# Optimization experiments

Measured on AMD Instinct MI355X. Metric: run time of the kernel, lower is better.

The kernel has to match this reference:

```python
import jax, jax.numpy as jnp
import numpy as np

N_ENT = 100000
N_REL = 500
D_IN = 128
D_OUT = 128
E_HALF = 1000000  # edges per direction; edge_index has 2*E_HALF columns
BN_EPS = 1e-5


def ccorr(a, b):
    # circular correlation: irfft(conj(rfft(a)) * rfft(b))
    d = a.shape[-1]
    return jnp.fft.irfft(jnp.conj(jnp.fft.rfft(a, axis=-1)) * jnp.fft.rfft(b, axis=-1), n=d, axis=-1)


def setup_inputs() -> dict:
    key = jax.random.key(0)
    ks = jax.random.split(key, 12)
    inv = 1.0 / np.sqrt(D_IN)
    inp = {
        "x": jax.random.normal(ks[0], (N_ENT, D_IN), dtype=jnp.float32),
        "rel_embed": jax.random.normal(ks[1], (N_REL, D_IN), dtype=jnp.float32),
        "w_in": jax.random.uniform(ks[2], (D_IN, D_OUT), minval=-inv, maxval=inv, dtype=jnp.float32),
        "w_out": jax.random.uniform(ks[3], (D_IN, D_OUT), minval=-inv, maxval=inv, dtype=jnp.float32),
        "w_loop": jax.random.uniform(ks[4], (D_IN, D_OUT), minval=-inv, maxval=inv, dtype=jnp.float32),
        "w_rel": jax.random.uniform(ks[5], (D_IN, D_OUT), minval=-inv, maxval=inv, dtype=jnp.float32),
        "loop_rel": jax.random.normal(ks[6], (1, D_IN), dtype=jnp.float32),
        "bias": jnp.zeros((D_OUT,), dtype=jnp.float32),
        "bn_weight": jnp.ones((D_OUT,), dtype=jnp.float32),
        "bn_bias": jnp.zeros((D_OUT,), dtype=jnp.float32),
        "edge_index": jax.random.randint(ks[7], (2, 2 * E_HALF), 0, N_ENT, dtype=jnp.int32),
        "edge_type": jax.random.randint(ks[8], (2 * E_HALF,), 0, N_REL, dtype=jnp.int32),
    }
    return inp


def _compute_norm(edge_index, num_ent):
    row, col = edge_index[0], edge_index[1]
    ones = jnp.ones(row.shape, dtype=jnp.float32)
    deg = jax.ops.segment_sum(ones, row, num_segments=num_ent)
    deg_inv = jnp.where(deg > 0, jax.lax.rsqrt(jnp.maximum(deg, 1.0)), 0.0)
    return deg_inv[row] * deg_inv[col]  # [E]


def _propagate(x, edge_index, edge_type, rel_all, weight, norm, num_ent):
    x_j = x[edge_index[0]]              # [E, d_in] gather source nodes
    r = rel_all[edge_type]              # [E, d_in] gather relation embeds
    m = ccorr(x_j, r) @ weight          # [E, d_out]
    if norm is not None:
        m = m * norm[:, None]
    return jax.ops.segment_sum(m, edge_index[1], num_segments=num_ent)


def reference(x, rel_embed, w_in, w_out, w_loop, w_rel, loop_rel, bias, bn_weight, bn_bias, edge_index, edge_type):
    num_ent = x.shape[0]
    rel_all = jnp.concatenate([rel_embed, loop_rel], axis=0)  # [R+1, d_in]
    e = edge_index.shape[1] // 2
    in_idx, out_idx = edge_index[:, :e], edge_index[:, e:]
    in_type, out_type = edge_type[:e], edge_type[e:]

    in_norm = _compute_norm(in_idx, num_ent)
    out_norm = _compute_norm(out_idx, num_ent)

    in_res = _propagate(x, in_idx, in_type, rel_all, w_in, in_norm, num_ent)
    out_res = _propagate(x, out_idx, out_type, rel_all, w_out, out_norm, num_ent)
    # loop edges are (i, i) with relation = last row of rel_all -> identity scatter
    loop_res = ccorr(x, rel_all[-1][None, :]) @ w_loop

    out = (in_res + out_res + loop_res) * (1.0 / 3.0) + bias
    # BatchNorm1d (training-mode batch statistics, biased variance)
    mu = jnp.mean(out, axis=0)
    var = jnp.mean((out - mu) ** 2, axis=0)
    out = (out - mu) * jax.lax.rsqrt(var + BN_EPS) * bn_weight + bn_bias

    rel_out = (rel_all @ w_rel)[:-1]
    return out, rel_out
```

## Files before the change

### kernel.cpp

```cpp
#include <hip/hip_runtime.h>
#include <cmath>

#define N_ENT 100000
#define EHALF 1000000
#define N_REL 500
#define NBUK 196
#define DPB 512
#define SCAP 7680
#define DCAP 6656

#ifndef M_PI
#define M_PI 3.14159265358979323846
#endif

typedef _Float16 f16x8 __attribute__((ext_vector_type(8)));
typedef _Float16 f16x4 __attribute__((ext_vector_type(4)));
typedef _Float16 f16x2 __attribute__((ext_vector_type(2)));
typedef float f32x4 __attribute__((ext_vector_type(4)));

union H16 { unsigned short u; _Float16 h; };

__global__ void k_tabs(float* __restrict__ Ftab, float* __restrict__ Gtab,
                       _Float16* __restrict__ FtabT) {
  int i = blockIdx.x * 256 + threadIdx.x;
  if (i >= 128 * 128) return;
  int n = i >> 7, s = i & 127;
  float fv, gv;
  if (s == 0) { fv = 1.f; gv = 1.f / 384.f; }
  else if (s == 1) { float sg = (n & 1) ? -1.f : 1.f; fv = sg; gv = sg / 384.f; }
  else {
    int f = s >> 1;
    double ang = 2.0 * M_PI * (double)((f * n) & 127) / 128.0;
    if (!(s & 1)) { double c = cos(ang); fv = (float)c; gv = (float)(c * (2.0 / 384.0)); }
    else { double sv = sin(ang); fv = (float)(-sv); gv = (float)(-sv * (2.0 / 384.0)); }
  }
  Ftab[n * 128 + s] = fv;
  Gtab[s * 128 + n] = gv;
  FtabT[s * 128 + n] = (_Float16)fv;
}

__global__ void k_dftrel(const float* __restrict__ rel, const float* __restrict__ looprel,
                         const float* __restrict__ Ftab, float* __restrict__ Rf,
                         _Float16* __restrict__ RfL) {
  __shared__ float sv[128];
  int r = blockIdx.x, s = threadIdx.x;
  const float* row = (r < N_REL) ? rel + (size_t)r * 128 : looprel;
  float acc = 0.f;
  for (int n = 0; n < 128; ++n) acc += row[n] * Ftab[n * 128 + s];
  Rf[(size_t)r * 128 + s] = acc;
  sv[s] = acc;
  __syncthreads();
  if (s < 64) {
    f16x4 o;
    if (s == 0) {
      o = (f16x4){(_Float16)sv[0], (_Float16)0.f, (_Float16)0.f, (_Float16)sv[1]};
    } else {
      float rx = sv[2 * s], ry = sv[2 * s + 1];
      o = (f16x4){(_Float16)rx, (_Float16)ry, (_Float16)ry, (_Float16)(-rx)};
    }
    ((f16x4*)RfL)[(size_t)r * 64 + s] = o;
  }
}

__global__ void k_rotloop(float* __restrict__ Wl, const float* __restrict__ Rfl) {
  int c = threadIdx.x;
  int f = blockIdx.x;
  if (f == 0) {
    Wl[c]       = Rfl[0] * Wl[c];
    Wl[128 + c] = Rfl[1] * Wl[128 + c];
  } else {
    float rr = Rfl[2 * f], ri = Rfl[2 * f + 1];
    float a = Wl[2 * f * 128 + c], b = Wl[(2 * f + 1) * 128 + c];
    Wl[2 * f * 128 + c]       = rr * a + ri * b;
    Wl[(2 * f + 1) * 128 + c] = ri * a - rr * b;
  }
}

__global__ void k_wt(const float* __restrict__ W, _Float16* __restrict__ WT, int K) {
  int i = blockIdx.x * 256 + threadIdx.x;
  if (i >= K * 128) return;
  int k = i >> 7, c = i & 127;
  WT[(size_t)c * K + k] = (_Float16)W[i];
}

__global__ __launch_bounds__(256) void gemm128(
    const float* __restrict__ A, int lda,
    const float* __restrict__ B,
    float* __restrict__ C, int ldc,
    int M, int K) {
  __shared__ float As[64][64];
  __shared__ float Bs[64][128];
  const int t = threadIdx.x;
  const int m0 = blockIdx.x * 64;
  const int cg = t & 31;
  const int eg = t >> 5;
  float acc[8][4];
#pragma unroll
  for (int i = 0; i < 8; ++i)
#pragma unroll
    for (int j = 0; j < 4; ++j) acc[i][j] = 0.f;

  for (int k0 = 0; k0 < K; k0 += 64) {
#pragma unroll
    for (int p = 0; p < 4; ++p) {
      int idx = t + p * 256;
      int r = idx >> 4, c4 = idx & 15;
      int gr = m0 + r;
      float4 v = make_float4(0.f, 0.f, 0.f, 0.f);
      if (gr < M) v = *(const float4*)(A + (size_t)gr * lda + k0 + c4 * 4);
      *(float4*)&As[r][c4 * 4] = v;
    }
#pragma unroll
    for (int p = 0; p < 8; ++p) {
      int idx = t + p * 256;
      int r = idx >> 5, c4 = idx & 31;
      float4 v = *(const float4*)(B + (size_t)(k0 + r) * 128 + c4 * 4);
      *(float4*)&Bs[r][c4 * 4] = v;
    }
    __syncthreads();
#pragma unroll
    for (int k = 0; k < 64; ++k) {
      float4 bv = *(float4*)&Bs[k][cg * 4];
#pragma unroll
      for (int i = 0; i < 8; ++i) {
        float av = As[eg * 8 + i][k];
        acc[i][0] += av * bv.x; acc[i][1] += av * bv.y;
        acc[i][2] += av * bv.z; acc[i][3] += av * bv.w;
      }
    }
    __syncthreads();
  }
#pragma unroll
  for (int i = 0; i < 8; ++i) {
    int gr = m0 + eg * 8 + i;
    if (gr < M) {
      float4 v = make_float4(acc[i][0], acc[i][1], acc[i][2], acc[i][3]);
      *(float4*)(C + (size_t)gr * ldc + cg * 4) = v;
    }
  }
}

__device__ inline f16x8 loadAfrag(const _Float16* A, size_t off) {
  return *(const f16x8*)(A + off);
}
__device__ inline f16x8 loadAfrag(const float* A, size_t off) {
  float4 u = *(const float4*)(A + off);
  float4 v = *(const float4*)(A + off + 4);
  return (f16x8){(_Float16)u.x, (_Float16)u.y, (_Float16)u.z, (_Float16)u.w,
                 (_Float16)v.x, (_Float16)v.y, (_Float16)v.z, (_Float16)v.w};
}

template<int K, int KS, int MODE, bool BN, typename AT>
__global__ __launch_bounds__(256) void mgemm(
    const AT* __restrict__ A, int lda,
    const _Float16* __restrict__ BT,
    void* __restrict__ Cv, int ldc, int M,
    const float* __restrict__ bias, float* __restrict__ bnAcc) {
  __shared__ __align__(16) char lds[128 * KS * 2 + 4096];
  const int t = threadIdx.x;
  const int l = t & 63, w = t >> 6;
  const int col0 = l & 15, rg = l >> 4;
  const int rowbase = blockIdx.x * 256 + w * 64;
  const int sw = (col0 & 7) << 4;

  f32x4 acc[4][8];
  f32x4 zz = {0.f, 0.f, 0.f, 0.f};
#pragma unroll
  for (int a = 0; a < 4; ++a)
#pragma unroll
    for (int n = 0; n < 8; ++n) acc[a][n] = zz;

  for (int ks0 = 0; ks0 < K; ks0 += KS) {
    __syncthreads();
    const int CH = KS / 8;
    for (int u = t; u < 128 * CH; u += 256) {
      int col = u / CH, kc = u % CH;
      f16x8 vch = *(const f16x8*)(BT + (size_t)col * K + ks0 + kc * 8);
      *(f16x8*)(lds + col * (KS * 2) + ((kc * 16) ^ ((col & 7) << 4))) = vch;
    }
    __syncthreads();
#pragma unroll
    for (int ks = 0; ks < KS / 32; ++ks) {
      int kb = ks0 + ks * 32 + rg * 8;
      f16x8 af[4];
#pragma unroll
      for (int a = 0; a < 4; ++a) {
        int rb = rowbase + a * 16;
        if (rb < M) af[a] = loadAfrag(A, (size_t)(rb + col0) * lda + kb);
        else af[a] = (f16x8){0, 0, 0, 0, 0, 0, 0, 0};
      }
      int kc = ks * 4 + rg;
#pragma unroll
      for (int n = 0; n < 8; ++n) {
        f16x8 bf = *(const f16x8*)(lds + (n * 16 + col0) * (KS * 2) + ((kc * 16) ^ sw));
#pragma unroll
        for (int a = 0; a < 4; ++a)
          acc[a][n] = __builtin_amdgcn_mfma_f32_16x16x32_f16(af[a], bf, acc[a][n], 0, 0, 0);
      }
    }
  }

  if (MODE == 1) {
    _Float16* C = (_Float16*)Cv;
#pragma unroll
    for (int a = 0; a < 4; ++a) {
      int rb = rowbase + a * 16;
      if (rb >= M) continue;
#pragma unroll
      for (int r = 0; r < 4; ++r) {
        int row = rb + rg * 4 + r;
#pragma unroll
        for (int n = 0; n < 8; ++n) {
          int col = n * 16 + col0;
          C[(size_t)row * ldc + col] = (_Float16)acc[a][n][r];
        }
      }
    }
  } else {
    float* C = (float*)Cv;
    float sacc[8], qacc[8];
#pragma unroll
    for (int n = 0; n < 8; ++n) { sacc[n] = 0.f; qacc[n] = 0.f; }
#pragma unroll
    for (int a = 0; a < 4; ++a) {
      int rb = rowbase + a * 16;
      if (rb >= M) continue;
#pragma unroll
      for (int n = 0; n < 8; ++n) {
        int col = n * 16 + col0;
        float bi = bias ? bias[col] : 0.f;
#pragma unroll
        for (int r = 0; r < 4; ++r) {
          float val = acc[a][n][r] + bi;
          C[(size_t)(rb + rg * 4 + r) * ldc + col] = val;
          if (BN) { sacc[n] += val; qacc[n] += val * val; }
        }
      }
    }
    if (BN) {
      __syncthreads();
      float* Sb = (float*)lds;
      float* Qb = Sb + 512;
#pragma unroll
      for (int n = 0; n < 8; ++n) {
        float s = sacc[n], q = qacc[n];
        s += __shfl_xor(s, 16); s += __shfl_xor(s, 32);
        q += __shfl_xor(q, 16); q += __shfl_xor(q, 32);
        if (rg == 0) { Sb[w * 128 + n * 16 + col0] = s; Qb[w * 128 + n * 16 + col0] = q; }
      }
      __syncthreads();
      if (t < 128) {
        float s = Sb[t] + Sb[128 + t] + Sb[256 + t] + Sb[384 + t];
        float q = Qb[t] + Qb[128 + t] + Qb[256 + t] + Qb[384 + t];
        atomicAdd(&bnAcc[t], s);
        atomicAdd(&bnAcc[128 + t], q);
      }
    }
  }
}

__global__ void k_init(int* __restrict__ gSI, int* __restrict__ gSO,
                       int* __restrict__ gDI, int* __restrict__ gDO) {
  int t = threadIdx.x;
  if (t < NBUK) {
    gSI[t] = t * SCAP; gSO[t] = t * SCAP;
    gDI[t] = t * DCAP; gDO[t] = t * DCAP;
  }
}

__global__ __launch_bounds__(256) void k_splitS2(
    const int* __restrict__ ei,
    int* __restrict__ gSI, int* __restrict__ gSO,
    unsigned* __restrict__ recSI, unsigned* __restrict__ recSO) {
  __shared__ int bcnt[NBUK], cnt2[NBUK], base[NBUK], nn[NBUK];
  const int t = threadIdx.x;
  const int dir = blockIdx.x >> 8;
  const int blk = blockIdx.x & 255;
  const int* key = ei + (dir ? EHALF : 0);
  int* gcur = dir ? gSO : gSI;
  unsigned* rec = dir ? recSO : recSI;
  const int SPAN = 3907;
  int st = blk * SPAN;
  int en = min(st + SPAN, EHALF);
  if (t < NBUK) { bcnt[t] = 0; cnt2[t] = 0; }
  __syncthreads();
  unsigned rr[16]; int bb[16];
#pragma unroll
  for (int j = 0; j < 16; ++j) {
    int e = st + j * 256 + t;
    bb[j] = -1;
    if (e < en) {
      int s = key[e];
      rr[j] = (unsigned)(s & 511) | 0x80000000u;
      int b = s >> 9;
      bb[j] = b;
      atomicAdd(&bcnt[b], 1);
    }
  }
  __syncthreads();
  if (t < NBUK) {
    int n = bcnt[t]; nn[t] = n;
    base[t] = n ? atomicAdd(&gcur[t], (n + 7) & ~7) : 0;
  }
  __syncthreads();
#pragma unroll
  for (int j = 0; j < 16; ++j) {
    if (bb[j] >= 0) {
      int p = atomicAdd(&cnt2[bb[j]], 1);
      rec[(size_t)base[bb[j]] + p] = rr[j];
    }
  }
  __syncthreads();
  if (t < NBUK) {
    int n = nn[t];
    if (n & 7) {
      int pe = (n + 7) & ~7;
      for (int k = n; k < pe; ++k) rec[(size_t)base[t] + k] = 0u;
    }
  }
}

__global__ __launch_bounds__(512) void k_dhist(
    const unsigned* __restrict__ recI, const int* __restrict__ gI,
    float* __restrict__ dinvIn,
    const unsigned* __restrict__ recO, const int* __restrict__ gO,
    float* __restrict__ dinvOut) {
  int b = blockIdx.x % NBUK;
  int dir = blockIdx.x / NBUK;
  const unsigned* rec = dir ? recO : recI;
  const int gs = b * SCAP;
  const int ge = (dir ? gO : gI)[b];
  float* dinv = dir ? dinvOut : dinvIn;
  __shared__ int h[DPB];
  int t = threadIdx.x;
  h[t] = 0;
  __syncthreads();
  for (int i = gs + t; i < ge; i += 512) {
    unsigned r = rec[i];
    if (r >> 31) atomicAdd(&h[r & 511], 1);
  }
  __syncthreads();
  int ent = b * 512 + t;
  if (ent < N_ENT) {
    int d = h[t];
    dinv[ent] = (d > 0) ? rsqrtf((float)d) : 0.f;
  }
}

__global__ __launch_bounds__(256) void k_splitD2(
    const int* __restrict__ ei, const int* __restrict__ et,
    const float* __restrict__ dinvIn, const float* __restrict__ dinvOut,
    int* __restrict__ gDI, int* __restrict__ gDO,
    uint2* __restrict__ recDI, uint2* __restrict__ recDO) {
  __shared__ int bcnt[NBUK], cnt2[NBUK], base[NBUK], nn[NBUK];
  const int t = threadIdx.x;
  const int dir = blockIdx.x >> 8;
  const int blk = blockIdx.x & 255;
  const int* srcA = ei + (dir ? EHALF : 0);
  const int* dstA = ei + (dir ? 3 * EHALF : 2 * EHALF);
  const int* typA = et + (dir ? EHALF : 0);
  const float* dv = dir ? dinvOut : dinvIn;
  int* gcur = dir ? gDO : gDI;
  uint2* rec = dir ? recDO : recDI;
  const int SPAN = 3907;
  int st = blk * SPAN;
  int en = min(st + SPAN, EHALF);
  if (t < NBUK) { bcnt[t] = 0; cnt2[t] = 0; }
  __syncthreads();
  unsigned w0[16], w1[16]; int bb[16];
#pragma unroll
  for (int j = 0; j < 16; ++j) {
    int e = st + j * 256 + t;
    bb[j] = -1;
    if (e < en) {
      int s = srcA[e], d = dstA[e], ty = typA[e];
      float nm = dv[s] * dv[d];
      H16 cv; cv.h = (_Float16)nm;
      w0[j] = (unsigned)s | ((unsigned)ty << 17);
      w1[j] = (unsigned)(d & 511) | ((unsigned)cv.u << 16);
      int b = d >> 9;
      bb[j] = b;
      atomicAdd(&bcnt[b], 1);
    }
  }
  __syncthreads();
  if (t < NBUK) {
    int n = bcnt[t]; nn[t] = n;
    base[t] = n ? atomicAdd(&gcur[t], (n + 3) & ~3) : 0;
  }
  __syncthreads();
#pragma unroll
  for (int j = 0; j < 16; ++j) {
    if (bb[j] >= 0) {
      int p = atomicAdd(&cnt2[bb[j]], 1);
      rec[(size_t)base[bb[j]] + p] = make_uint2(w0[j], w1[j]);
    }
  }
  __syncthreads();
  if (t < NBUK) {
    int n = nn[t];
    if (n & 3) {
      int pe = (n + 3) & ~3;
      for (int k = n; k < pe; ++k) rec[(size_t)base[t] + k] = make_uint2(0u, 0u);
    }
  }
}

__global__ __launch_bounds__(512) void k_fsort(
    const uint2* __restrict__ recDI, const int* __restrict__ gDI,
    uint2* __restrict__ csrIn, int2* __restrict__ beI,
    const uint2* __restrict__ recDO, const int* __restrict__ gDO,
    uint2* __restrict__ csrOut, int2* __restrict__ beO) {
  int b = blockIdx.x % NBUK;
  int dir = blockIdx.x / NBUK;
  const uint2* rec = dir ? recDO : recDI;
  const int gs = b * DCAP;
  const int ge = (dir ? gDO : gDI)[b];
  uint2* csr = dir ? csrOut : csrIn;
  int2* be = dir ? beO : beI;
  __shared__ int h[DPB], sc[DPB], c2[DPB];
  int t = threadIdx.x;
  h[t] = 0; c2[t] = 0;
  __syncthreads();
  for (int i = gs + t; i < ge; i += 512) {
    uint2 r = rec[i];
    if (r.y >> 16) atomicAdd(&h[r.y & 511], 1);
  }
  __syncthreads();
  sc[t] = h[t];
  __syncthreads();
  for (int o = 1; o < 512; o <<= 1) {
    int a = (t >= o) ? sc[t - o] : 0;
    __syncthreads();
    sc[t] += a;
    __syncthreads();
  }
  int excl = sc[t] - h[t];
  int ent = b * 512 + t;
  if (ent < N_ENT) be[ent] = make_int2(gs + excl, gs + excl + h[t]);
  __syncthreads();
  sc[t] = excl;
  __syncthreads();
  for (int i = gs + t; i < ge; i += 512) {
    uint2 r = rec[i];
    if (r.y >> 16) {
      int d = r.y & 511;
      int p = atomicAdd(&c2[d], 1);
      csr[(size_t)gs + sc[d] + p] =
          make_uint2(((r.x & 0x1FFFFu) * 3u) << 8,
                     (r.x >> 17) | (r.y & 0xFFFF0000u));
    }
  }
}

__device__ inline void estep(uint2 q, const char* __restrict__ Xb,
                             const char* __restrict__ Rb,
                             unsigned lxc, unsigned lr, float& ax, float& ay) {
  f16x2 xv = *(const f16x2*)(Xb + q.x + lxc);
  f16x4 rv = *(const f16x4*)(Rb + ((q.y & 0x1FFu) << 9) + lr);
  H16 nu; nu.u = (unsigned short)(q.y >> 16);
  float nm = (float)nu.h;
  float px = fmaf((float)xv[0], (float)rv[0], (float)xv[1] * (float)rv[1]);
  float py = fmaf((float)xv[0], (float)rv[2], (float)xv[1] * (float)rv[3]);
  ax = fmaf(nm, px, ax);
  ay = fmaf(nm, py, ay);
}

__global__ __launch_bounds__(256) void k_agg(
    _Float16* __restrict__ Abuf, const _Float16* __restrict__ RfL,
    const uint2* __restrict__ csrIn, const int2* __restrict__ beI,
    const uint2* __restrict__ csrOut, const int2* __restrict__ beO) {
  const int w = threadIdx.x >> 6, l = threadIdx.x & 63;
  const int v = blockIdx.x * 4 + w;
  const char* Xb = (const char*)Abuf;
  const char* Rb = (const char*)RfL;
  const unsigned lxc = 512u + (unsigned)l * 4u;
  const unsigned lr = (unsigned)l * 8u;
  int2 bi = beI[v], bo = beO[v];
  int i = bi.x, ie = bi.y;
  int o = bo.x, oe = bo.y;
  float aix = 0.f, aiy = 0.f, aox = 0.f, aoy = 0.f;

  while (i + 4 <= ie && o + 4 <= oe) {
    uint2 a0 = csrIn[i], a1 = csrIn[i + 1], a2 = csrIn[i + 2], a3 = csrIn[i + 3];
    uint2 b0 = csrOut[o], b1 = csrOut[o + 1], b2 = csrOut[o + 2], b3 = csrOut[o + 3];
    estep(a0, Xb, Rb, lxc, lr, aix, aiy);
    estep(b0, Xb, Rb, lxc, lr, aox, aoy);
    estep(a1, Xb, Rb, lxc, lr, aix, aiy);
    estep(b1, Xb, Rb, lxc, lr, aox, aoy);
    estep(a2, Xb, Rb, lxc, lr, aix, aiy);
    estep(b2, Xb, Rb, lxc, lr, aox, aoy);
    estep(a3, Xb, Rb, lxc, lr, aix, aiy);
    estep(b3, Xb, Rb, lxc, lr, aox, aoy);
    i += 4; o += 4;
  }
  while (i + 4 <= ie) {
    uint2 a0 = csrIn[i], a1 = csrIn[i + 1], a2 = csrIn[i + 2], a3 = csrIn[i + 3];
    estep(a0, Xb, Rb, lxc, lr, aix, aiy);
    estep(a1, Xb, Rb, lxc, lr, aix, aiy);
    estep(a2, Xb, Rb, lxc, lr, aix, aiy);
    estep(a3, Xb, Rb, lxc, lr, aix, aiy);
    i += 4;
  }
  while (o + 4 <= oe) {
    uint2 b0 = csrOut[o], b1 = csrOut[o + 1], b2 = csrOut[o + 2], b3 = csrOut[o + 3];
    estep(b0, Xb, Rb, lxc, lr, aox, aoy);
    estep(b1, Xb, Rb, lxc, lr, aox, aoy);
    estep(b2, Xb, Rb, lxc, lr, aox, aoy);
    estep(b3, Xb, Rb, lxc, lr, aox, aoy);
    o += 4;
  }
  while (i < ie) { estep(csrIn[i], Xb, Rb, lxc, lr, aix, aiy); ++i; }
  while (o < oe) { estep(csrOut[o], Xb, Rb, lxc, lr, aox, aoy); ++o; }

  *(f16x2*)((char*)Abuf + (size_t)v * 768 + 4u * l) = (f16x2){(_Float16)aix, (_Float16)aiy};
  *(f16x2*)((char*)Abuf + (size_t)v * 768 + 256 + 4u * l) = (f16x2){(_Float16)aox, (_Float16)aoy};
}

__global__ void k_bnfin(const float* __restrict__ bnAcc, const float* __restrict__ bnw,
                        const float* __restrict__ bnb, float* __restrict__ ss) {
  int c = threadIdx.x;
  float mu = bnAcc[c] * (1.f / (float)N_ENT);
  float var = bnAcc[128 + c] * (1.f / (float)N_ENT) - mu * mu;
  float sc = bnw[c] * rsqrtf(var + 1e-5f);
  ss[c] = sc; ss[128 + c] = bnb[c] - mu * sc;
}

__global__ void k_norm(float* __restrict__ out, const float* __restrict__ ss) {
  int i = blockIdx.x * 256 + threadIdx.x;
  float4* o = (float4*)out;
  float4 v = o[i];
  int c = (i & 31) * 4;
  v.x = v.x * ss[c]     + ss[128 + c];
  v.y = v.y * ss[c + 1] + ss[129 + c];
  v.z = v.z * ss[c + 2] + ss[130 + c];
  v.w = v.w * ss[c + 3] + ss[131 + c];
  o[i] = v;
}

extern "C" void kernel_launch(void* const* d_in, const int* in_sizes, int n_in,
                              void* d_out, int out_size, void* d_ws, size_t ws_size,
                              hipStream_t stream) {
  const float* x       = (const float*)d_in[0];
  const float* rel     = (const float*)d_in[1];
  const float* w_in    = (const float*)d_in[2];
  const float* w_out   = (const float*)d_in[3];
  const float* w_loop  = (const float*)d_in[4];
  const float* w_rel   = (const float*)d_in[5];
  const float* looprel = (const float*)d_in[6];
  const float* bias    = (const float*)d_in[7];
  const float* bnw     = (const float*)d_in[8];
  const float* bnb     = (const float*)d_in[9];
  const int*   ei      = (const int*)d_in[10];
  const int*   et      = (const int*)d_in[11];
  float* out = (float*)d_out;

  char* p = (char*)d_ws;
  auto alloc = [&](size_t bytes) -> void* {
    void* r = (void*)p;
    p += (bytes + 255) & ~(size_t)255;
    return r;
  };
  _Float16* Abuf  = (_Float16*)alloc((size_t)N_ENT * 384 * 2);
  _Float16* WT    = (_Float16*)alloc(128 * 384 * 2);
  _Float16* FtabT = (_Float16*)alloc(128 * 128 * 2);
  _Float16* RfL   = (_Float16*)alloc(501 * 64 * 4 * 2);
  float* Wstack   = (float*)alloc(384 * 128 * 4);
  float* Ftab     = (float*)alloc(128 * 128 * 4);
  float* Gtab     = (float*)alloc(128 * 128 * 4);
  float* Rf       = (float*)alloc(501 * 128 * 4);
  float* dinvIn   = (float*)alloc(N_ENT * 4);
  float* dinvOut  = (float*)alloc(N_ENT * 4);
  int*   gSI      = (int*)alloc(NBUK * 4);
  int*   gSO      = (int*)alloc(NBUK * 4);
  int*   gDI      = (int*)alloc(NBUK * 4);
  int*   gDO      = (int*)alloc(NBUK * 4);
  int2*  beI      = (int2*)alloc((size_t)N_ENT * 8);
  int2*  beO      = (int2*)alloc((size_t)N_ENT * 8);
  unsigned* recSI = (unsigned*)alloc((size_t)NBUK * SCAP * 4);
  unsigned* recSO = (unsigned*)alloc((size_t)NBUK * SCAP * 4);
  uint2* recDI    = (uint2*)alloc((size_t)NBUK * DCAP * 8);
  uint2* recDO    = (uint2*)alloc((size_t)NBUK * DCAP * 8);
  uint2* csrIn    = (uint2*)alloc((size_t)NBUK * DCAP * 8);
  uint2* csrOut   = (uint2*)alloc((size_t)NBUK * DCAP * 8);
  float* bnAcc    = (float*)alloc(256 * 4);
  float* ss       = (float*)alloc(256 * 4);

  hipMemsetAsync(bnAcc, 0, 256 * 4, stream);

  k_tabs<<<64, 256, 0, stream>>>(Ftab, Gtab, FtabT);
  k_dftrel<<<501, 128, 0, stream>>>(rel, looprel, Ftab, Rf, RfL);
  gemm128<<<2, 256, 0, stream>>>(Gtab, 128, w_in,   Wstack,             128, 128, 128);
  gemm128<<<2, 256, 0, stream>>>(Gtab, 128, w_out,  Wstack + 128 * 128, 128, 128, 128);
  gemm128<<<2, 256, 0, stream>>>(Gtab, 128, w_loop, Wstack + 256 * 128, 128, 128, 128);
  k_rotloop<<<64, 128, 0, stream>>>(Wstack + 256 * 128, Rf + 500 * 128);
  k_wt<<<192, 256, 0, stream>>>(Wstack, WT, 384);

  mgemm<128, 128, 1, false, float><<<(N_ENT + 255) / 256, 256, 0, stream>>>(
      x, 128, FtabT, (void*)(Abuf + 256), 384, N_ENT, nullptr, nullptr);

  k_init<<<1, 256, 0, stream>>>(gSI, gSO, gDI, gDO);
  k_splitS2<<<512, 256, 0, stream>>>(ei, gSI, gSO, recSI, recSO);
  k_dhist<<<2 * NBUK, 512, 0, stream>>>(recSI, gSI, dinvIn, recSO, gSO, dinvOut);
  k_splitD2<<<512, 256, 0, stream>>>(ei, et, dinvIn, dinvOut, gDI, gDO, recDI, recDO);
  k_fsort<<<2 * NBUK, 512, 0, stream>>>(recDI, gDI, csrIn, beI, recDO, gDO, csrOut, beO);

  k_agg<<<N_ENT / 4, 256, 0, stream>>>(Abuf, RfL, csrIn, beI, csrOut, beO);

  mgemm<384, 192, 0, true, _Float16><<<(N_ENT + 255) / 256, 256, 0, stream>>>(
      Abuf, 384, WT, (void*)out, 128, N_ENT, bias, bnAcc);
  k_bnfin<<<1, 128, 0, stream>>>(bnAcc, bnw, bnb, ss);
  k_norm<<<(N_ENT * 128 / 4) / 256, 256, 0, stream>>>(out, ss);

  gemm128<<<(N_REL + 63) / 64, 256, 0, stream>>>(rel, 128, w_rel, out + (size_t)N_ENT * 128, 128, N_REL, 128);
}
```

Measured before the change: 359.7 us.

## Store pre-BN output in fp16, use fdot2 in aggregation, merge setup launches

The final GEMM now writes its biased pre-normalization result to an fp16 scratch buffer, and the normalize kernel reads that buffer and writes fp32 output, cutting intermediate memory traffic. The aggregation inner step pre-scales the gathered fp16 features by the edge norm and uses packed fp16 dot2 instructions instead of scalar fp32 FMAs. Setup launches are consolidated: three tiny weight GEMMs become one kernel, the loop rotation is folded into the transpose kernel, and the counter-init kernel is replaced by a memset with bucket offsets added at use. The risk is reduced accuracy from fp16 rounding of the pre-BN output and from the fp16 products of feature and norm.

```diff
diff --git a/kernel.cpp b/kernel.cpp
--- a/kernel.cpp
+++ b/kernel.cpp
@@ -19,6 +19,7 @@
 typedef float f32x4 __attribute__((ext_vector_type(4)));
 
 union H16 { unsigned short u; _Float16 h; };
+union HU32 { unsigned u; f16x2 h; };
 
 __global__ void k_tabs(float* __restrict__ Ftab, float* __restrict__ Gtab,
                        _Float16* __restrict__ FtabT) {
@@ -62,36 +63,36 @@
   }
 }
 
-__global__ void k_rotloop(float* __restrict__ Wl, const float* __restrict__ Rfl) {
-  int c = threadIdx.x;
-  int f = blockIdx.x;
-  if (f == 0) {
-    Wl[c]       = Rfl[0] * Wl[c];
-    Wl[128 + c] = Rfl[1] * Wl[128 + c];
+__global__ void k_wt(const float* __restrict__ W, const float* __restrict__ Rfl,
+                     _Float16* __restrict__ WT) {
+  int i = blockIdx.x * 256 + threadIdx.x;
+  if (i >= 384 * 128) return;
+  int k = i >> 7, c = i & 127;
+  float val;
+  if (k < 256) {
+    val = W[i];
   } else {
-    float rr = Rfl[2 * f], ri = Rfl[2 * f + 1];
-    float a = Wl[2 * f * 128 + c], b = Wl[(2 * f + 1) * 128 + c];
-    Wl[2 * f * 128 + c]       = rr * a + ri * b;
-    Wl[(2 * f + 1) * 128 + c] = ri * a - rr * b;
-  }
-}
-
-__global__ void k_wt(const float* __restrict__ W, _Float16* __restrict__ WT, int K) {
-  int i = blockIdx.x * 256 + threadIdx.x;
-  if (i >= K * 128) return;
-  int k = i >> 7, c = i & 127;
-  WT[(size_t)c * K + k] = (_Float16)W[i];
-}
-
-__global__ __launch_bounds__(256) void gemm128(
-    const float* __restrict__ A, int lda,
-    const float* __restrict__ B,
-    float* __restrict__ C, int ldc,
-    int M, int K) {
+    int kk = k - 256;
+    if (kk == 0)      val = Rfl[0] * W[i];
+    else if (kk == 1) val = Rfl[1] * W[i];
+    else {
+      int f = kk >> 1;
+      float rr = Rfl[2 * f], ri = Rfl[2 * f + 1];
+      float a = W[(256 + 2 * f) * 128 + c];
+      float b = W[(256 + 2 * f + 1) * 128 + c];
+      val = (kk & 1) ? (ri * a - rr * b) : (rr * a + ri * b);
+    }
+  }
+  WT[(size_t)c * 384 + k] = (_Float16)val;
+}
+
+__device__ void gemm128_body(const float* __restrict__ A, int lda,
+                             const float* __restrict__ B,
+                             float* __restrict__ C, int ldc,
+                             int M, int K, int m0) {
   __shared__ float As[64][64];
   __shared__ float Bs[64][128];
   const int t = threadIdx.x;
-  const int m0 = blockIdx.x * 64;
   const int cg = t & 31;
   const int eg = t >> 5;
   float acc[8][4];
@@ -140,6 +141,22 @@
   }
 }
 
+__global__ __launch_bounds__(256) void gemm128(
+    const float* __restrict__ A, int lda, const float* __restrict__ B,
+    float* __restrict__ C, int ldc, int M, int K) {
+  gemm128_body(A, lda, B, C, ldc, M, K, blockIdx.x * 64);
+}
+
+__global__ __launch_bounds__(256) void k_wprep(
+    const float* __restrict__ Gtab, const float* __restrict__ w0,
+    const float* __restrict__ w1, const float* __restrict__ w2,
+    float* __restrict__ Wstack) {
+  int which = blockIdx.x >> 1;
+  const float* B = (which == 0) ? w0 : ((which == 1) ? w1 : w2);
+  gemm128_body(Gtab, 128, B, Wstack + which * 128 * 128, 128, 128, 128,
+               (blockIdx.x & 1) * 64);
+}
+
 __device__ inline f16x8 loadAfrag(const _Float16* A, size_t off) {
   return *(const f16x8*)(A + off);
 }
@@ -150,11 +167,11 @@
                  (_Float16)v.x, (_Float16)v.y, (_Float16)v.z, (_Float16)v.w};
 }
 
-template<int K, int KS, int MODE, bool BN, typename AT>
+template<int K, int KS, int MODE, typename AT>
 __global__ __launch_bounds__(256) void mgemm(
     const AT* __restrict__ A, int lda,
     const _Float16* __restrict__ BT,
-    void* __restrict__ Cv, int ldc, int M,
+    _Float16* __restrict__ C, int ldc, int M,
     const float* __restrict__ bias, float* __restrict__ bnAcc) {
   __shared__ __align__(16) char lds[128 * KS * 2 + 4096];
   const int t = threadIdx.x;
@@ -201,7 +218,6 @@
   }
 
   if (MODE == 1) {
-    _Float16* C = (_Float16*)Cv;
 #pragma unroll
     for (int a = 0; a < 4; ++a) {
       int rb = rowbase + a * 16;
@@ -217,7 +233,6 @@
       }
     }
   } else {
-    float* C = (float*)Cv;
     float sacc[8], qacc[8];
 #pragma unroll
     for (int n = 0; n < 8; ++n) { sacc[n] = 0.f; qacc[n] = 0.f; }
@@ -228,43 +243,32 @@
 #pragma unroll
       for (int n = 0; n < 8; ++n) {
         int col = n * 16 + col0;
-        float bi = bias ? bias[col] : 0.f;
+        float bi = bias[col];
 #pragma unroll
         for (int r = 0; r < 4; ++r) {
           float val = acc[a][n][r] + bi;
-          C[(size_t)(rb + rg * 4 + r) * ldc + col] = val;
-          if (BN) { sacc[n] += val; qacc[n] += val * val; }
+          C[(size_t)(rb + rg * 4 + r) * ldc + col] = (_Float16)val;
+          sacc[n] += val; qacc[n] += val * val;
         }
       }
     }
-    if (BN) {
-      __syncthreads();
-      float* Sb = (float*)lds;
-      float* Qb = Sb + 512;
-#pragma unroll
-      for (int n = 0; n < 8; ++n) {
-        float s = sacc[n], q = qacc[n];
-        s += __shfl_xor(s, 16); s += __shfl_xor(s, 32);
-        q += __shfl_xor(q, 16); q += __shfl_xor(q, 32);
-        if (rg == 0) { Sb[w * 128 + n * 16 + col0] = s; Qb[w * 128 + n * 16 + col0] = q; }
-      }
-      __syncthreads();
-      if (t < 128) {
-        float s = Sb[t] + Sb[128 + t] + Sb[256 + t] + Sb[384 + t];
-        float q = Qb[t] + Qb[128 + t] + Qb[256 + t] + Qb[384 + t];
-        atomicAdd(&bnAcc[t], s);
-        atomicAdd(&bnAcc[128 + t], q);
-      }
-    }
-  }
-}
-
-__global__ void k_init(int* __restrict__ gSI, int* __restrict__ gSO,
-                       int* __restrict__ gDI, int* __restrict__ gDO) {
-  int t = threadIdx.x;
-  if (t < NBUK) {
-    gSI[t] = t * SCAP; gSO[t] = t * SCAP;
-    gDI[t] = t * DCAP; gDO[t] = t * DCAP;
+    __syncthreads();
+    float* Sb = (float*)lds;
+    float* Qb = Sb + 512;
+#pragma unroll
+    for (int n = 0; n < 8; ++n) {
+      float s = sacc[n], q = qacc[n];
+      s += __shfl_xor(s, 16); s += __shfl_xor(s, 32);
+      q += __shfl_xor(q, 16); q += __shfl_xor(q, 32);
+      if (rg == 0) { Sb[w * 128 + n * 16 + col0] = s; Qb[w * 128 + n * 16 + col0] = q; }
+    }
+    __syncthreads();
+    if (t < 128) {
+      float s = Sb[t] + Sb[128 + t] + Sb[256 + t] + Sb[384 + t];
+      float q = Qb[t] + Qb[128 + t] + Qb[256 + t] + Qb[384 + t];
+      atomicAdd(&bnAcc[t], s);
+      atomicAdd(&bnAcc[128 + t], q);
+    }
   }
 }
 
@@ -300,7 +304,7 @@
   __syncthreads();
   if (t < NBUK) {
     int n = bcnt[t]; nn[t] = n;
-    base[t] = n ? atomicAdd(&gcur[t], (n + 7) & ~7) : 0;
+    base[t] = n ? (t * SCAP + atomicAdd(&gcur[t], (n + 7) & ~7)) : 0;
   }
   __syncthreads();
 #pragma unroll
@@ -329,7 +333,7 @@
   int dir = blockIdx.x / NBUK;
   const unsigned* rec = dir ? recO : recI;
   const int gs = b * SCAP;
-  const int ge = (dir ? gO : gI)[b];
+  const int ge = gs + (dir ? gO : gI)[b];
   float* dinv = dir ? dinvOut : dinvIn;
   __shared__ int h[DPB];
   int t = threadIdx.x;
@@ -386,7 +390,7 @@
   __syncthreads();
   if (t < NBUK) {
     int n = bcnt[t]; nn[t] = n;
-    base[t] = n ? atomicAdd(&gcur[t], (n + 3) & ~3) : 0;
+    base[t] = n ? (t * DCAP + atomicAdd(&gcur[t], (n + 3) & ~3)) : 0;
   }
   __syncthreads();
 #pragma unroll
@@ -415,7 +419,7 @@
   int dir = blockIdx.x / NBUK;
   const uint2* rec = dir ? recDO : recDI;
   const int gs = b * DCAP;
-  const int ge = (dir ? gDO : gDI)[b];
+  const int ge = gs + (dir ? gDO : gDI)[b];
   uint2* csr = dir ? csrOut : csrIn;
   int2* be = dir ? beO : beI;
   __shared__ int h[DPB], sc[DPB], c2[DPB];
@@ -453,17 +457,24 @@
   }
 }
 
+__device__ inline float dot2f(f16x2 a, f16x2 b, float c) {
+#if __has_builtin(__builtin_amdgcn_fdot2)
+  return __builtin_amdgcn_fdot2(a, b, c, false);
+#else
+  return fmaf((float)a[0], (float)b[0], fmaf((float)a[1], (float)b[1], c));
+#endif
+}
+
 __device__ inline void estep(uint2 q, const char* __restrict__ Xb,
                              const char* __restrict__ Rb,
                              unsigned lxc, unsigned lr, float& ax, float& ay) {
   f16x2 xv = *(const f16x2*)(Xb + q.x + lxc);
   f16x4 rv = *(const f16x4*)(Rb + ((q.y & 0x1FFu) << 9) + lr);
-  H16 nu; nu.u = (unsigned short)(q.y >> 16);
-  float nm = (float)nu.h;
-  float px = fmaf((float)xv[0], (float)rv[0], (float)xv[1] * (float)rv[1]);
-  float py = fmaf((float)xv[0], (float)rv[2], (float)xv[1] * (float)rv[3]);
-  ax = fmaf(nm, px, ax);
-  ay = fmaf(nm, py, ay);
+  HU32 nm; nm.u = (q.y >> 16) | (q.y & 0xFFFF0000u);
+  f16x2 xs = xv * nm.h;
+  f16x2 rlo = {rv[0], rv[1]}, rhi = {rv[2], rv[3]};
+  ax = dot2f(xs, rlo, ax);
+  ay = dot2f(xs, rhi, ay);
 }
 
 __global__ __launch_bounds__(256) void k_agg(
@@ -526,16 +537,22 @@
   ss[c] = sc; ss[128 + c] = bnb[c] - mu * sc;
 }
 
-__global__ void k_norm(float* __restrict__ out, const float* __restrict__ ss) {
+__global__ void k_norm(const _Float16* __restrict__ tmp, float* __restrict__ out,
+                       const float* __restrict__ ss) {
   int i = blockIdx.x * 256 + threadIdx.x;
-  float4* o = (float4*)out;
-  float4 v = o[i];
-  int c = (i & 31) * 4;
-  v.x = v.x * ss[c]     + ss[128 + c];
-  v.y = v.y * ss[c + 1] + ss[129 + c];
-  v.z = v.z * ss[c + 2] + ss[130 + c];
-  v.w = v.w * ss[c + 3] + ss[131 + c];
-  o[i] = v;
+  f16x8 v = ((const f16x8*)tmp)[i];
+  int cb = (i & 15) * 8;
+  float4 o0, o1;
+  o0.x = (float)v[0] * ss[cb]     + ss[128 + cb];
+  o0.y = (float)v[1] * ss[cb + 1] + ss[129 + cb];
+  o0.z = (float)v[2] * ss[cb + 2] + ss[130 + cb];
+  o0.w = (float)v[3] * ss[cb + 3] + ss[131 + cb];
+  o1.x = (float)v[4] * ss[cb + 4] + ss[132 + cb];
+  o1.y = (float)v[5] * ss[cb + 5] + ss[133 + cb];
+  o1.z = (float)v[6] * ss[cb + 6] + ss[134 + cb];
+  o1.w = (float)v[7] * ss[cb + 7] + ss[135 + cb];
+  ((float4*)out)[2 * i] = o0;
+  ((float4*)out)[2 * i + 1] = o1;
 }
 
 extern "C" void kernel_launch(void* const* d_in, const int* in_sizes, int n_in,
@@ -562,6 +579,7 @@
     return r;
   };
   _Float16* Abuf  = (_Float16*)alloc((size_t)N_ENT * 384 * 2);
+  _Float16* tmpC  = (_Float16*)alloc((size_t)N_ENT * 128 * 2);
   _Float16* WT    = (_Float16*)alloc(128 * 384 * 2);
   _Float16* FtabT = (_Float16*)alloc(128 * 128 * 2);
   _Float16* RfL   = (_Float16*)alloc(501 * 64 * 4 * 2);
@@ -571,10 +589,7 @@
   float* Rf       = (float*)alloc(501 * 128 * 4);
   float* dinvIn   = (float*)alloc(N_ENT * 4);
   float* dinvOut  = (float*)alloc(N_ENT * 4);
-  int*   gSI      = (int*)alloc(NBUK * 4);
-  int*   gSO      = (int*)alloc(NBUK * 4);
-  int*   gDI      = (int*)alloc(NBUK * 4);
-  int*   gDO      = (int*)alloc(NBUK * 4);
+  int*   gcur     = (int*)alloc(4 * NBUK * 4);
   int2*  beI      = (int2*)alloc((size_t)N_ENT * 8);
   int2*  beO      = (int2*)alloc((size_t)N_ENT * 8);
   unsigned* recSI = (unsigned*)alloc((size_t)NBUK * SCAP * 4);
@@ -586,20 +601,22 @@
   float* bnAcc    = (float*)alloc(256 * 4);
   float* ss       = (float*)alloc(256 * 4);
 
+  int* gSI = gcur;
+  int* gSO = gcur + NBUK;
+  int* gDI = gcur + 2 * NBUK;
+  int* gDO = gcur + 3 * NBUK;
+
+  hipMemsetAsync(gcur, 0, 4 * NBUK * 4, stream);
   hipMemsetAsync(bnAcc, 0, 256 * 4, stream);
 
   k_tabs<<<64, 256, 0, stream>>>(Ftab, Gtab, FtabT);
   k_dftrel<<<501, 128, 0, stream>>>(rel, looprel, Ftab, Rf, RfL);
-  gemm128<<<2, 256, 0, stream>>>(Gtab, 128, w_in,   Wstack,             128, 128, 128);
-  gemm128<<<2, 256, 0, stream>>>(Gtab, 128, w_out,  Wstack + 128 * 128, 128, 128, 128);
-  gemm128<<<2, 256, 0, stream>>>(Gtab, 128, w_loop, Wstack + 256 * 128, 128, 128, 128);
-  k_rotloop<<<64, 128, 0, stream>>>(Wstack + 256 * 128, Rf + 500 * 128);
-  k_wt<<<192, 256, 0, stream>>>(Wstack, WT, 384);
-
-  mgemm<128, 128, 1, false, float><<<(N_ENT + 255) / 256, 256, 0, stream>>>(
-      x, 128, FtabT, (void*)(Abuf + 256), 384, N_ENT, nullptr, nullptr);
-
-  k_init<<<1, 256, 0, stream>>>(gSI, gSO, gDI, gDO);
+  k_wprep<<<6, 256, 0, stream>>>(Gtab, w_in, w_out, w_loop, Wstack);
+  k_wt<<<192, 256, 0, stream>>>(Wstack, Rf + 500 * 128, WT);
+
+  mgemm<128, 128, 1, float><<<(N_ENT + 255) / 256, 256, 0, stream>>>(
+      x, 128, FtabT, Abuf + 256, 384, N_ENT, nullptr, nullptr);
+
   k_splitS2<<<512, 256, 0, stream>>>(ei, gSI, gSO, recSI, recSO);
   k_dhist<<<2 * NBUK, 512, 0, stream>>>(recSI, gSI, dinvIn, recSO, gSO, dinvOut);
   k_splitD2<<<512, 256, 0, stream>>>(ei, et, dinvIn, dinvOut, gDI, gDO, recDI, recDO);
@@ -607,10 +624,10 @@
 
   k_agg<<<N_ENT / 4, 256, 0, stream>>>(Abuf, RfL, csrIn, beI, csrOut, beO);
 
-  mgemm<384, 192, 0, true, _Float16><<<(N_ENT + 255) / 256, 256, 0, stream>>>(
-      Abuf, 384, WT, (void*)out, 128, N_ENT, bias, bnAcc);
+  mgemm<384, 192, 2, _Float16><<<(N_ENT + 255) / 256, 256, 0, stream>>>(
+      Abuf, 384, WT, tmpC, 128, N_ENT, bias, bnAcc);
   k_bnfin<<<1, 128, 0, stream>>>(bnAcc, bnw, bnb, ss);
-  k_norm<<<(N_ENT * 128 / 4) / 256, 256, 0, stream>>>(out, ss);
+  k_norm<<<(N_ENT * 128 / 8) / 256, 256, 0, stream>>>(tmpC, out, ss);
 
   gemm128<<<(N_REL + 63) / 64, 256, 0, stream>>>(rel, 128, w_rel, out + (size_t)N_ENT * 128, 128, N_REL, 128);
 }
```

Result: faster. 337.1 us (-6.3%).
